# Kernel tuning notes

Hardware: AMD Instinct MI355X
Metric: run time of the kernel (lower is better)

The kernel has to match this reference:

```python
import jax, jax.numpy as jnp
import numpy as np

N_NODES = 100000
FEAT = 256
MAX_DEG = 128
BATCH = 1024
# sampler k uses layer_infos[num_layers-1-k].num_samples: layer_infos num_samples = [25, 10]
NUM_SAMPLES_PER_HOP = [10, 25]
DEPTH = 2


def setup_inputs() -> dict:
    key = jax.random.key(0)
    ks = jax.random.split(key, 10)
    s = 0.05
    return {
        "features": jax.random.normal(ks[0], (N_NODES, FEAT), jnp.float32),
        "w_self_0": jax.random.normal(ks[3], (FEAT, 128), jnp.float32) * s,
        "w_neigh_0": jax.random.normal(ks[4], (FEAT, 128), jnp.float32) * s,
        "w_self_1": jax.random.normal(ks[5], (256, 128), jnp.float32) * s,  # in = 2*128 concat
        "w_neigh_1": jax.random.normal(ks[6], (256, 128), jnp.float32) * s,
        "w_out": jax.random.normal(ks[7], (256, 1), jnp.float32) * s,
        "b_out": jnp.zeros((1,), jnp.float32),
        "node_ids": jax.random.randint(ks[2], (BATCH,), 0, N_NODES, jnp.int32),
        "adj": jax.random.randint(ks[1], (N_NODES, MAX_DEG), 0, N_NODES, jnp.int32),
    }


def _sample(node_ids, adj):
    """Multi-hop uniform neighbor sampling (UniformNeighborSampler chain)."""
    skey = jax.random.key(42)
    samples = [node_ids.reshape(-1)]
    for k, ns in enumerate(NUM_SAMPLES_PER_HOP):
        ids = samples[k]
        rows = jnp.take(adj, ids, axis=0)  # [M, MAX_DEG]
        cols = jax.random.randint(jax.random.fold_in(skey, k), (ids.shape[0], ns), 0, adj.shape[1])
        samples.append(jnp.take_along_axis(rows, cols, axis=1).reshape(-1))
    return samples


def reference(features, w_self_0, w_neigh_0, w_self_1, w_neigh_1, w_out, b_out, node_ids, adj):
    samples = _sample(node_ids, adj)
    hidden = [jnp.take(features, s, axis=0) for s in samples]
    params = [(w_self_0, w_neigh_0), (w_self_1, w_neigh_1)]
    for k in range(DEPTH):
        w_s, w_n = params[k]
        next_hidden = []
        for hop in range(DEPTH - k):
            self_v = hidden[hop]                                   # [M, d]
            neigh = hidden[hop + 1].reshape(self_v.shape[0], NUM_SAMPLES_PER_HOP[hop], -1)
            neigh_mean = neigh.mean(axis=1)                        # [M, d]
            # MeanAggregator, concat=True: relu(concat(self@Ws, mean@Wn))
            next_hidden.append(jax.nn.relu(jnp.concatenate([self_v @ w_s, neigh_mean @ w_n], axis=1)))
        hidden = next_hidden
    h = hidden[0]                                                  # [BATCH, 256]
    h = h / jnp.sqrt(jnp.maximum(jnp.sum(h * h, axis=1, keepdims=True), 1e-12))  # l2_normalize
    return h @ w_out + b_out                                       # Dense(1)
```

## Files before the change

### kernel.cpp

```cpp
#include <hip/hip_runtime.h>
#include <math.h>

struct K2 { unsigned a, b; };

__host__ __device__ constexpr unsigned rotl32c(unsigned x, int r) {
  return (x << r) | (x >> (32 - r));
}

__host__ __device__ constexpr K2 threefry2x32(unsigned k0, unsigned k1,
                                              unsigned x0, unsigned x1) {
  const unsigned ks2 = k0 ^ k1 ^ 0x1BD11BDAu;
  const unsigned ks[3] = {k0, k1, ks2};
  const int rotA[4] = {13, 15, 26, 6};
  const int rotB[4] = {17, 29, 16, 24};
  x0 += k0; x1 += k1;
  for (int g = 0; g < 5; ++g) {
    const int* rr = (g & 1) ? rotB : rotA;
    for (int i = 0; i < 4; ++i) {
      x0 += x1;
      x1 = rotl32c(x1, rr[i]);
      x1 ^= x0;
    }
    x0 += ks[(g + 1) % 3];
    x1 += ks[(g + 2) % 3] + (unsigned)(g + 1);
  }
  return K2{x0, x1};
}

__host__ __device__ constexpr K2 hop_key(unsigned k) {
  K2 f = threefry2x32(0u, 42u, 0u, k);
  return threefry2x32(f.a, f.b, 0u, 1u);
}

constexpr K2 HK0 = hop_key(0u);
constexpr K2 HK1 = hop_key(1u);

__global__ __launch_bounds__(256) void sample_hop1(
    const int* __restrict__ ids, const int* __restrict__ adj,
    int* __restrict__ out, int n) {
  int i = blockIdx.x * 256 + threadIdx.x;
  if (i >= n) return;
  K2 r = threefry2x32(HK0.a, HK0.b, 0u, (unsigned)i);
  int col = (int)((r.a ^ r.b) & 127u);
  out[i] = adj[(long long)ids[i / 10] * 128 + col];
}

__global__ __launch_bounds__(256) void sample_mean_hop2(
    const int* __restrict__ s1, const int* __restrict__ adj,
    const float* __restrict__ feat, float* __restrict__ dst) {
  const int m = blockIdx.x * 4 + (threadIdx.x >> 6);
  const int lane = threadIdx.x & 63;

  const int nid = s1[m];
  int srow;
  {
    unsigned i = (unsigned)(m * 25 + (lane < 25 ? lane : 0));
    K2 r = threefry2x32(HK1.a, HK1.b, 0u, i);
    int col = (int)((r.a ^ r.b) & 127u);
    srow = adj[(long long)nid * 128 + col];
  }

  float4 acc = make_float4(0.f, 0.f, 0.f, 0.f);
#pragma unroll
  for (int c = 0; c < 25; c += 5) {
    float4 v[5];
#pragma unroll
    for (int j = 0; j < 5; ++j) {
      long long row = (long long)__shfl(srow, c + j, 64);
      v[j] = *(const float4*)(feat + row * 256 + (lane << 2));
    }
#pragma unroll
    for (int j = 0; j < 5; ++j) {
      acc.x += v[j].x; acc.y += v[j].y; acc.z += v[j].z; acc.w += v[j].w;
    }
  }
  const float invS = 1.f / 25.f;
  acc.x *= invS; acc.y *= invS; acc.z *= invS; acc.w *= invS;
  *(float4*)(dst + (long long)m * 256 + (lane << 2)) = acc;
}

template <int S>
__global__ __launch_bounds__(256) void mean_rows_w(
    const float* __restrict__ src, const int* __restrict__ idx,
    float* __restrict__ dst, float invS) {
  const int m = blockIdx.x * 4 + (threadIdx.x >> 6);
  const int lane = threadIdx.x & 63;
  const long long base = (long long)m * S;

  int srow = 0;
  if (idx) srow = idx[base + (lane < S ? lane : 0)];

  float4 acc = make_float4(0.f, 0.f, 0.f, 0.f);
#pragma unroll
  for (int c = 0; c < S; c += 5) {
    float4 v[5];
#pragma unroll
    for (int j = 0; j < 5; ++j) {
      if (c + j < S) {
        long long row = idx ? (long long)__shfl(srow, c + j, 64) : (base + c + j);
        v[j] = *(const float4*)(src + row * 256 + (lane << 2));
      }
    }
#pragma unroll
    for (int j = 0; j < 5; ++j) {
      if (c + j < S) {
        acc.x += v[j].x; acc.y += v[j].y; acc.z += v[j].z; acc.w += v[j].w;
      }
    }
  }
  acc.x *= invS; acc.y *= invS; acc.z *= invS; acc.w *= invS;
  *(float4*)(dst + (long long)m * 256 + (lane << 2)) = acc;
}

struct GemmCfg {
  const float* A; const int* idx; const float* B; float* C;
  int ccol0; int mtiles;
};
struct GemmCfg4 { GemmCfg c[4]; };

__global__ __launch_bounds__(256) void gemm_relu_multi(GemmCfg4 cfgs) {
  const GemmCfg cfg = cfgs.c[blockIdx.z];
  if ((int)blockIdx.x >= cfg.mtiles) return;

  __shared__ __align__(16) float As[16][68];
  __shared__ __align__(16) float Bs[16][68];

  const int t = threadIdx.x;
  const int tx = t & 15, ty = t >> 4;
  const int brow = blockIdx.x * 64;
  const int bcol = blockIdx.y * 64;

  const int arow = t >> 2;
  const int ak4 = (t & 3) << 2;
  const int grow = brow + arow;
  const long long asrc = cfg.idx ? (long long)cfg.idx[grow] : (long long)grow;
  const float* Ap = cfg.A + asrc * 256 + ak4;
  const float* Bp = cfg.B + (t >> 4) * 128 + bcol + ((t & 15) << 2);
  const int bkk = t >> 4;
  const int bn4 = (t & 15) << 2;

  float acc[4][4] = {{0.f}};

  for (int k0 = 0; k0 < 256; k0 += 16) {
    float4 av = *(const float4*)(Ap + k0);
    float4 bv = *(const float4*)(Bp + (long long)k0 * 128);
    __syncthreads();
    As[ak4 + 0][arow] = av.x;
    As[ak4 + 1][arow] = av.y;
    As[ak4 + 2][arow] = av.z;
    As[ak4 + 3][arow] = av.w;
    Bs[bkk][bn4 + 0] = bv.x;
    Bs[bkk][bn4 + 1] = bv.y;
    Bs[bkk][bn4 + 2] = bv.z;
    Bs[bkk][bn4 + 3] = bv.w;
    __syncthreads();
#pragma unroll
    for (int kk = 0; kk < 16; ++kk) {
      float4 a = *(const float4*)&As[kk][ty << 2];
      float4 b = *(const float4*)&Bs[kk][tx << 2];
      acc[0][0] += a.x * b.x; acc[0][1] += a.x * b.y; acc[0][2] += a.x * b.z; acc[0][3] += a.x * b.w;
      acc[1][0] += a.y * b.x; acc[1][1] += a.y * b.y; acc[1][2] += a.y * b.z; acc[1][3] += a.y * b.w;
      acc[2][0] += a.z * b.x; acc[2][1] += a.z * b.y; acc[2][2] += a.z * b.z; acc[2][3] += a.z * b.w;
      acc[3][0] += a.w * b.x; acc[3][1] += a.w * b.y; acc[3][2] += a.w * b.z; acc[3][3] += a.w * b.w;
    }
  }

#pragma unroll
  for (int i = 0; i < 4; ++i) {
    const int r = brow + (ty << 2) + i;
    float* Cp = cfg.C + (long long)r * 256 + cfg.ccol0 + bcol + (tx << 2);
#pragma unroll
    for (int j = 0; j < 4; ++j) {
      float v = acc[i][j];
      Cp[j] = v > 0.f ? v : 0.f;
    }
  }
}

__global__ __launch_bounds__(256) void final_kernel(
    const float* __restrict__ h, const float* __restrict__ w,
    const float* __restrict__ b, float* __restrict__ out) {
  const int m = blockIdx.x;
  const int t = threadIdx.x;
  float v = h[(long long)m * 256 + t];
  float wv = w[t];
  float ss = v * v;
  float dd = v * wv;
  for (int off = 32; off; off >>= 1) {
    ss += __shfl_down(ss, off, 64);
    dd += __shfl_down(dd, off, 64);
  }
  __shared__ float s1[4], s2[4];
  const int wid = t >> 6, lane = t & 63;
  if (lane == 0) { s1[wid] = ss; s2[wid] = dd; }
  __syncthreads();
  if (t == 0) {
    float S = s1[0] + s1[1] + s1[2] + s1[3];
    float D = s2[0] + s2[1] + s2[2] + s2[3];
    float n = sqrtf(fmaxf(S, 1e-12f));
    out[m] = D / n + b[0];
  }
}

extern "C" void kernel_launch(void* const* d_in, const int* in_sizes, int n_in,
                              void* d_out, int out_size, void* d_ws, size_t ws_size,
                              hipStream_t stream) {
  (void)in_sizes; (void)n_in; (void)out_size; (void)ws_size;

  const float* features  = (const float*)d_in[0];
  const float* w_self_0  = (const float*)d_in[1];
  const float* w_neigh_0 = (const float*)d_in[2];
  const float* w_self_1  = (const float*)d_in[3];
  const float* w_neigh_1 = (const float*)d_in[4];
  const float* w_out     = (const float*)d_in[5];
  const float* b_out     = (const float*)d_in[6];
  const int*   node_ids  = (const int*)d_in[7];
  const int*   adj       = (const int*)d_in[8];
  float* out = (float*)d_out;

  char* ws = (char*)d_ws;
  size_t off = 0;
  auto alloc = [&](size_t bytes) -> void* {
    void* p = ws + off;
    off = (off + bytes + 255) & ~(size_t)255;
    return p;
  };
  int*   s1   = (int*)alloc(10240 * sizeof(int));
  float* nm1  = (float*)alloc((size_t)10240 * 256 * 4);
  float* nm0  = (float*)alloc((size_t)1024 * 256 * 4);
  float* out1 = (float*)alloc((size_t)10240 * 256 * 4);
  float* out0 = (float*)alloc((size_t)1024 * 256 * 4);
  float* nml1 = (float*)alloc((size_t)1024 * 256 * 4);
  float* hbuf = (float*)alloc((size_t)1024 * 256 * 4);

  sample_hop1<<<40, 256, 0, stream>>>(node_ids, adj, s1, 10240);

  sample_mean_hop2<<<2560, 256, 0, stream>>>(s1, adj, features, nm1);
  mean_rows_w<10><<<256, 256, 0, stream>>>(features, s1, nm0, 0.1f);

  {
    GemmCfg4 cf;
    cf.c[0] = {features, s1,       w_self_0,  out1, 0,   160};
    cf.c[1] = {nm1,      nullptr,  w_neigh_0, out1, 128, 160};
    cf.c[2] = {features, node_ids, w_self_0,  out0, 0,   16};
    cf.c[3] = {nm0,      nullptr,  w_neigh_0, out0, 128, 16};
    gemm_relu_multi<<<dim3(160, 2, 4), 256, 0, stream>>>(cf);
  }

  mean_rows_w<10><<<256, 256, 0, stream>>>(out1, nullptr, nml1, 0.1f);
  {
    GemmCfg4 cf;
    cf.c[0] = {out0, nullptr, w_self_1,  hbuf, 0,   16};
    cf.c[1] = {nml1, nullptr, w_neigh_1, hbuf, 128, 16};
    cf.c[2] = {nullptr, nullptr, nullptr, nullptr, 0, 0};
    cf.c[3] = {nullptr, nullptr, nullptr, nullptr, 0, 0};
    gemm_relu_multi<<<dim3(16, 2, 2), 256, 0, stream>>>(cf);
  }

  final_kernel<<<1024, 256, 0, stream>>>(hbuf, w_out, b_out, out);
}
```

Measured before the change: 253.2 us.

## Template GEMM tiles, use 128x128 tiles with register prefetch and flattened grid

The fused GEMM kernel is templated on block and thread tile sizes. The big first-layer GEMMs move to 128x128 tiles with 8x8 per-thread outputs, the second layer keeps 64x64. Global loads for the next k-slice are now prefetched into registers while the current slice is computed. The 3D grid is replaced by a flat grid that is split across problem configs, so no blocks exit early. Larger tiles raise data reuse and arithmetic intensity, but they use more registers and give fewer blocks (176) than the GPU's CU count, which risks underfilling the device.

```diff
diff --git a/kernel.cpp b/kernel.cpp
--- a/kernel.cpp
+++ b/kernel.cpp
@@ -114,63 +114,93 @@
 
 struct GemmCfg {
   const float* A; const int* idx; const float* B; float* C;
-  int ccol0; int mtiles;
+  int ccol0; int mtiles; int ntiles;
 };
 struct GemmCfg4 { GemmCfg c[4]; };
 
+template <int BM, int BN, int TM, int TN>
 __global__ __launch_bounds__(256) void gemm_relu_multi(GemmCfg4 cfgs) {
-  const GemmCfg cfg = cfgs.c[blockIdx.z];
-  if ((int)blockIdx.x >= cfg.mtiles) return;
-
-  __shared__ __align__(16) float As[16][68];
-  __shared__ __align__(16) float Bs[16][68];
+  int b = blockIdx.x;
+  int z = 0;
+  while (z < 3 && b >= cfgs.c[z].ntiles) { b -= cfgs.c[z].ntiles; ++z; }
+  const GemmCfg cfg = cfgs.c[z];
+  const int mt = b % cfg.mtiles;
+  const int nt = b / cfg.mtiles;
+
+  __shared__ __align__(16) float As[16][BM + 4];
+  __shared__ __align__(16) float Bs[16][BN + 4];
 
   const int t = threadIdx.x;
   const int tx = t & 15, ty = t >> 4;
-  const int brow = blockIdx.x * 64;
-  const int bcol = blockIdx.y * 64;
-
-  const int arow = t >> 2;
-  const int ak4 = (t & 3) << 2;
-  const int grow = brow + arow;
+
+  constexpr int A4 = BM / 64;
+  constexpr int B4 = BN / 64;
+
+  int arow, akb;
+  if constexpr (BM == 128) { arow = t >> 1; akb = (t & 1) << 3; }
+  else { arow = t >> 2; akb = (t & 3) << 2; }
+  const int grow = mt * BM + arow;
   const long long asrc = cfg.idx ? (long long)cfg.idx[grow] : (long long)grow;
-  const float* Ap = cfg.A + asrc * 256 + ak4;
-  const float* Bp = cfg.B + (t >> 4) * 128 + bcol + ((t & 15) << 2);
+  const float* Ap = cfg.A + asrc * 256 + akb;
+
   const int bkk = t >> 4;
-  const int bn4 = (t & 15) << 2;
-
-  float acc[4][4] = {{0.f}};
+  const int bnb = (t & 15) * (BN / 16);
+  const float* Bp = cfg.B + bkk * 128 + nt * BN + bnb;
+
+  float4 av[A4], bv[B4];
+#pragma unroll
+  for (int u = 0; u < A4; ++u) av[u] = *(const float4*)(Ap + (u << 2));
+#pragma unroll
+  for (int u = 0; u < B4; ++u) bv[u] = *(const float4*)(Bp + (u << 2));
+
+  float acc[TM][TN] = {};
 
   for (int k0 = 0; k0 < 256; k0 += 16) {
-    float4 av = *(const float4*)(Ap + k0);
-    float4 bv = *(const float4*)(Bp + (long long)k0 * 128);
     __syncthreads();
-    As[ak4 + 0][arow] = av.x;
-    As[ak4 + 1][arow] = av.y;
-    As[ak4 + 2][arow] = av.z;
-    As[ak4 + 3][arow] = av.w;
-    Bs[bkk][bn4 + 0] = bv.x;
-    Bs[bkk][bn4 + 1] = bv.y;
-    Bs[bkk][bn4 + 2] = bv.z;
-    Bs[bkk][bn4 + 3] = bv.w;
+#pragma unroll
+    for (int u = 0; u < A4; ++u) {
+      As[akb + (u << 2) + 0][arow] = av[u].x;
+      As[akb + (u << 2) + 1][arow] = av[u].y;
+      As[akb + (u << 2) + 2][arow] = av[u].z;
+      As[akb + (u << 2) + 3][arow] = av[u].w;
+    }
+#pragma unroll
+    for (int u = 0; u < B4; ++u)
+      *(float4*)&Bs[bkk][bnb + (u << 2)] = bv[u];
     __syncthreads();
+
+    if (k0 + 16 < 256) {
+#pragma unroll
+      for (int u = 0; u < A4; ++u)
+        av[u] = *(const float4*)(Ap + k0 + 16 + (u << 2));
+#pragma unroll
+      for (int u = 0; u < B4; ++u)
+        bv[u] = *(const float4*)(Bp + (long long)(k0 + 16) * 128 + (u << 2));
+    }
+
 #pragma unroll
     for (int kk = 0; kk < 16; ++kk) {
-      float4 a = *(const float4*)&As[kk][ty << 2];
-      float4 b = *(const float4*)&Bs[kk][tx << 2];
-      acc[0][0] += a.x * b.x; acc[0][1] += a.x * b.y; acc[0][2] += a.x * b.z; acc[0][3] += a.x * b.w;
-      acc[1][0] += a.y * b.x; acc[1][1] += a.y * b.y; acc[1][2] += a.y * b.z; acc[1][3] += a.y * b.w;
-      acc[2][0] += a.z * b.x; acc[2][1] += a.z * b.y; acc[2][2] += a.z * b.z; acc[2][3] += a.z * b.w;
-      acc[3][0] += a.w * b.x; acc[3][1] += a.w * b.y; acc[3][2] += a.w * b.z; acc[3][3] += a.w * b.w;
-    }
-  }
-
-#pragma unroll
-  for (int i = 0; i < 4; ++i) {
-    const int r = brow + (ty << 2) + i;
-    float* Cp = cfg.C + (long long)r * 256 + cfg.ccol0 + bcol + (tx << 2);
-#pragma unroll
-    for (int j = 0; j < 4; ++j) {
+      float a[TM], bb[TN];
+#pragma unroll
+      for (int u = 0; u < TM; u += 4)
+        *(float4*)&a[u] = *(const float4*)&As[kk][ty * TM + u];
+#pragma unroll
+      for (int u = 0; u < TN; u += 4)
+        *(float4*)&bb[u] = *(const float4*)&Bs[kk][tx * TN + u];
+#pragma unroll
+      for (int i = 0; i < TM; ++i)
+#pragma unroll
+        for (int j = 0; j < TN; ++j)
+          acc[i][j] += a[i] * bb[j];
+    }
+  }
+
+#pragma unroll
+  for (int i = 0; i < TM; ++i) {
+    const int r = mt * BM + ty * TM + i;
+    float* Cp = cfg.C + (long long)r * 256 + cfg.ccol0 + nt * BN + tx * TN;
+#pragma unroll
+    for (int j = 0; j < TN; ++j) {
       float v = acc[i][j];
       Cp[j] = v > 0.f ? v : 0.f;
     }
@@ -240,21 +270,21 @@
 
   {
     GemmCfg4 cf;
-    cf.c[0] = {features, s1,       w_self_0,  out1, 0,   160};
-    cf.c[1] = {nm1,      nullptr,  w_neigh_0, out1, 128, 160};
-    cf.c[2] = {features, node_ids, w_self_0,  out0, 0,   16};
-    cf.c[3] = {nm0,      nullptr,  w_neigh_0, out0, 128, 16};
-    gemm_relu_multi<<<dim3(160, 2, 4), 256, 0, stream>>>(cf);
+    cf.c[0] = {features, s1,       w_self_0,  out1, 0,   80, 80};
+    cf.c[1] = {nm1,      nullptr,  w_neigh_0, out1, 128, 80, 80};
+    cf.c[2] = {features, node_ids, w_self_0,  out0, 0,   8,  8};
+    cf.c[3] = {nm0,      nullptr,  w_neigh_0, out0, 128, 8,  8};
+    gemm_relu_multi<128, 128, 8, 8><<<176, 256, 0, stream>>>(cf);
   }
 
   mean_rows_w<10><<<256, 256, 0, stream>>>(out1, nullptr, nml1, 0.1f);
   {
     GemmCfg4 cf;
-    cf.c[0] = {out0, nullptr, w_self_1,  hbuf, 0,   16};
-    cf.c[1] = {nml1, nullptr, w_neigh_1, hbuf, 128, 16};
-    cf.c[2] = {nullptr, nullptr, nullptr, nullptr, 0, 0};
-    cf.c[3] = {nullptr, nullptr, nullptr, nullptr, 0, 0};
-    gemm_relu_multi<<<dim3(16, 2, 2), 256, 0, stream>>>(cf);
+    cf.c[0] = {out0, nullptr, w_self_1,  hbuf, 0,   16, 32};
+    cf.c[1] = {nml1, nullptr, w_neigh_1, hbuf, 128, 16, 32};
+    cf.c[2] = {nullptr, nullptr, nullptr, nullptr, 0, 1, 0};
+    cf.c[3] = {nullptr, nullptr, nullptr, nullptr, 0, 1, 0};
+    gemm_relu_multi<64, 64, 4, 4><<<64, 256, 0, stream>>>(cf);
   }
 
   final_kernel<<<1024, 256, 0, stream>>>(hbuf, w_out, b_out, out);
```

After: 264.4 us. 1.04x slower.

## Fuse sampling kernels, atomic-mean GEMM epilogue, fused final layer

Applied to the files above, without the earlier changes.

Merges hop-1 sampling, the hop-2 gather-mean and the hop-0 mean into one kernel that also zeroes the layer-1 neighbor-mean buffer. The big layer-0 GEMM now averages its outputs straight into that buffer with scaled atomicAdds, so the out1 intermediate and the separate mean pass are gone. The layer-1 GEMM, l2-normalize and output dot are fused into one kernel, and the GEMM grid is flattened into a 1-D tile list. This removes launches and a 10 MB intermediate round-trip. In exchange it adds atomic contention and order-dependent float sums, and the final kernel runs only 64 blocks.

```diff
diff --git a/kernel.cpp b/kernel.cpp
--- a/kernel.cpp
+++ b/kernel.cpp
@@ -35,111 +35,105 @@
 constexpr K2 HK0 = hop_key(0u);
 constexpr K2 HK1 = hop_key(1u);
 
-__global__ __launch_bounds__(256) void sample_hop1(
-    const int* __restrict__ ids, const int* __restrict__ adj,
-    int* __restrict__ out, int n) {
-  int i = blockIdx.x * 256 + threadIdx.x;
-  if (i >= n) return;
-  K2 r = threefry2x32(HK0.a, HK0.b, 0u, (unsigned)i);
-  int col = (int)((r.a ^ r.b) & 127u);
-  out[i] = adj[(long long)ids[i / 10] * 128 + col];
-}
-
-__global__ __launch_bounds__(256) void sample_mean_hop2(
-    const int* __restrict__ s1, const int* __restrict__ adj,
-    const float* __restrict__ feat, float* __restrict__ dst) {
-  const int m = blockIdx.x * 4 + (threadIdx.x >> 6);
+__global__ __launch_bounds__(256) void sample_means(
+    const int* __restrict__ node_ids, const int* __restrict__ adj,
+    const float* __restrict__ feat, int* __restrict__ s1,
+    float* __restrict__ nm1, float* __restrict__ nm0,
+    float* __restrict__ nml1) {
+  const int blk = blockIdx.x;
+  const int w = threadIdx.x >> 6;
   const int lane = threadIdx.x & 63;
 
-  const int nid = s1[m];
-  int srow;
-  {
-    unsigned i = (unsigned)(m * 25 + (lane < 25 ? lane : 0));
-    K2 r = threefry2x32(HK1.a, HK1.b, 0u, i);
-    int col = (int)((r.a ^ r.b) & 127u);
-    srow = adj[(long long)nid * 128 + col];
-  }
-
-  float4 acc = make_float4(0.f, 0.f, 0.f, 0.f);
-#pragma unroll
-  for (int c = 0; c < 25; c += 5) {
-    float4 v[5];
-#pragma unroll
-    for (int j = 0; j < 5; ++j) {
-      long long row = (long long)__shfl(srow, c + j, 64);
-      v[j] = *(const float4*)(feat + row * 256 + (lane << 2));
-    }
-#pragma unroll
-    for (int j = 0; j < 5; ++j) {
-      acc.x += v[j].x; acc.y += v[j].y; acc.z += v[j].z; acc.w += v[j].w;
-    }
-  }
-  const float invS = 1.f / 25.f;
-  acc.x *= invS; acc.y *= invS; acc.z *= invS; acc.w *= invS;
-  *(float4*)(dst + (long long)m * 256 + (lane << 2)) = acc;
-}
-
-template <int S>
-__global__ __launch_bounds__(256) void mean_rows_w(
-    const float* __restrict__ src, const int* __restrict__ idx,
-    float* __restrict__ dst, float invS) {
-  const int m = blockIdx.x * 4 + (threadIdx.x >> 6);
-  const int lane = threadIdx.x & 63;
-  const long long base = (long long)m * S;
-
-  int srow = 0;
-  if (idx) srow = idx[base + (lane < S ? lane : 0)];
-
-  float4 acc = make_float4(0.f, 0.f, 0.f, 0.f);
-#pragma unroll
-  for (int c = 0; c < S; c += 5) {
-    float4 v[5];
-#pragma unroll
-    for (int j = 0; j < 5; ++j) {
-      if (c + j < S) {
-        long long row = idx ? (long long)__shfl(srow, c + j, 64) : (base + c + j);
-        v[j] = *(const float4*)(src + row * 256 + (lane << 2));
-      }
-    }
-#pragma unroll
-    for (int j = 0; j < 5; ++j) {
-      if (c + j < S) {
+  if (blk < 256) {
+    ((float4*)nml1)[blk * 256 + threadIdx.x] = make_float4(0.f, 0.f, 0.f, 0.f);
+  }
+
+  if (blk < 2560) {
+    const int m = blk * 4 + w;
+    K2 r0 = threefry2x32(HK0.a, HK0.b, 0u, (unsigned)m);
+    const int nid = adj[(long long)node_ids[m / 10] * 128 +
+                        (int)((r0.a ^ r0.b) & 127u)];
+    if (lane == 0) s1[m] = nid;
+    int srow;
+    {
+      unsigned i = (unsigned)(m * 25 + (lane < 25 ? lane : 0));
+      K2 r = threefry2x32(HK1.a, HK1.b, 0u, i);
+      srow = adj[(long long)nid * 128 + (int)((r.a ^ r.b) & 127u)];
+    }
+    float4 acc = make_float4(0.f, 0.f, 0.f, 0.f);
+#pragma unroll
+    for (int c = 0; c < 25; c += 5) {
+      float4 v[5];
+#pragma unroll
+      for (int j = 0; j < 5; ++j) {
+        long long row = (long long)__shfl(srow, c + j, 64);
+        v[j] = *(const float4*)(feat + row * 256 + (lane << 2));
+      }
+#pragma unroll
+      for (int j = 0; j < 5; ++j) {
         acc.x += v[j].x; acc.y += v[j].y; acc.z += v[j].z; acc.w += v[j].w;
       }
     }
-  }
-  acc.x *= invS; acc.y *= invS; acc.z *= invS; acc.w *= invS;
-  *(float4*)(dst + (long long)m * 256 + (lane << 2)) = acc;
+    const float s = 1.f / 25.f;
+    acc.x *= s; acc.y *= s; acc.z *= s; acc.w *= s;
+    *(float4*)(nm1 + (long long)m * 256 + (lane << 2)) = acc;
+  } else {
+    const int m0 = (blk - 2560) * 4 + w;
+    int srow;
+    {
+      int j = lane < 10 ? lane : 0;
+      K2 r = threefry2x32(HK0.a, HK0.b, 0u, (unsigned)(m0 * 10 + j));
+      srow = adj[(long long)node_ids[m0] * 128 + (int)((r.a ^ r.b) & 127u)];
+    }
+    float4 acc = make_float4(0.f, 0.f, 0.f, 0.f);
+#pragma unroll
+    for (int c = 0; c < 10; c += 5) {
+      float4 v[5];
+#pragma unroll
+      for (int j = 0; j < 5; ++j) {
+        long long row = (long long)__shfl(srow, c + j, 64);
+        v[j] = *(const float4*)(feat + row * 256 + (lane << 2));
+      }
+#pragma unroll
+      for (int j = 0; j < 5; ++j) {
+        acc.x += v[j].x; acc.y += v[j].y; acc.z += v[j].z; acc.w += v[j].w;
+      }
+    }
+    acc.x *= 0.1f; acc.y *= 0.1f; acc.z *= 0.1f; acc.w *= 0.1f;
+    *(float4*)(nm0 + (long long)m0 * 256 + (lane << 2)) = acc;
+  }
 }
 
 struct GemmCfg {
   const float* A; const int* idx; const float* B; float* C;
-  int ccol0; int mtiles;
+  int ccol0; int mtiles; int tiles; int mode;
 };
 struct GemmCfg4 { GemmCfg c[4]; };
 
 __global__ __launch_bounds__(256) void gemm_relu_multi(GemmCfg4 cfgs) {
-  const GemmCfg cfg = cfgs.c[blockIdx.z];
-  if ((int)blockIdx.x >= cfg.mtiles) return;
+  int b = blockIdx.x, z = 0;
+  while (z < 3 && b >= cfgs.c[z].tiles) { b -= cfgs.c[z].tiles; ++z; }
+  const GemmCfg cfg = cfgs.c[z];
+  const int mt = b % cfg.mtiles;
+  const int nt = b / cfg.mtiles;
 
   __shared__ __align__(16) float As[16][68];
   __shared__ __align__(16) float Bs[16][68];
 
   const int t = threadIdx.x;
   const int tx = t & 15, ty = t >> 4;
-  const int brow = blockIdx.x * 64;
-  const int bcol = blockIdx.y * 64;
 
   const int arow = t >> 2;
   const int ak4 = (t & 3) << 2;
-  const int grow = brow + arow;
+  const int grow = mt * 64 + arow;
   const long long asrc = cfg.idx ? (long long)cfg.idx[grow] : (long long)grow;
   const float* Ap = cfg.A + asrc * 256 + ak4;
-  const float* Bp = cfg.B + (t >> 4) * 128 + bcol + ((t & 15) << 2);
+
   const int bkk = t >> 4;
   const int bn4 = (t & 15) << 2;
-
-  float acc[4][4] = {{0.f}};
+  const float* Bp = cfg.B + bkk * 128 + nt * 64 + bn4;
+
+  float acc[4][4] = {};
 
   for (int k0 = 0; k0 < 256; k0 += 16) {
     float4 av = *(const float4*)(Ap + k0);
@@ -149,56 +143,121 @@
     As[ak4 + 1][arow] = av.y;
     As[ak4 + 2][arow] = av.z;
     As[ak4 + 3][arow] = av.w;
-    Bs[bkk][bn4 + 0] = bv.x;
-    Bs[bkk][bn4 + 1] = bv.y;
-    Bs[bkk][bn4 + 2] = bv.z;
-    Bs[bkk][bn4 + 3] = bv.w;
+    *(float4*)&Bs[bkk][bn4] = bv;
     __syncthreads();
 #pragma unroll
     for (int kk = 0; kk < 16; ++kk) {
       float4 a = *(const float4*)&As[kk][ty << 2];
-      float4 b = *(const float4*)&Bs[kk][tx << 2];
-      acc[0][0] += a.x * b.x; acc[0][1] += a.x * b.y; acc[0][2] += a.x * b.z; acc[0][3] += a.x * b.w;
-      acc[1][0] += a.y * b.x; acc[1][1] += a.y * b.y; acc[1][2] += a.y * b.z; acc[1][3] += a.y * b.w;
-      acc[2][0] += a.z * b.x; acc[2][1] += a.z * b.y; acc[2][2] += a.z * b.z; acc[2][3] += a.z * b.w;
-      acc[3][0] += a.w * b.x; acc[3][1] += a.w * b.y; acc[3][2] += a.w * b.z; acc[3][3] += a.w * b.w;
-    }
-  }
-
-#pragma unroll
-  for (int i = 0; i < 4; ++i) {
-    const int r = brow + (ty << 2) + i;
-    float* Cp = cfg.C + (long long)r * 256 + cfg.ccol0 + bcol + (tx << 2);
-#pragma unroll
-    for (int j = 0; j < 4; ++j) {
-      float v = acc[i][j];
-      Cp[j] = v > 0.f ? v : 0.f;
-    }
-  }
-}
-
-__global__ __launch_bounds__(256) void final_kernel(
-    const float* __restrict__ h, const float* __restrict__ w,
-    const float* __restrict__ b, float* __restrict__ out) {
-  const int m = blockIdx.x;
+      float4 b4 = *(const float4*)&Bs[kk][tx << 2];
+      acc[0][0] += a.x * b4.x; acc[0][1] += a.x * b4.y; acc[0][2] += a.x * b4.z; acc[0][3] += a.x * b4.w;
+      acc[1][0] += a.y * b4.x; acc[1][1] += a.y * b4.y; acc[1][2] += a.y * b4.z; acc[1][3] += a.y * b4.w;
+      acc[2][0] += a.z * b4.x; acc[2][1] += a.z * b4.y; acc[2][2] += a.z * b4.z; acc[2][3] += a.z * b4.w;
+      acc[3][0] += a.w * b4.x; acc[3][1] += a.w * b4.y; acc[3][2] += a.w * b4.z; acc[3][3] += a.w * b4.w;
+    }
+  }
+
+  if (cfg.mode == 0) {
+#pragma unroll
+    for (int i = 0; i < 4; ++i) {
+      const int r = mt * 64 + (ty << 2) + i;
+      float* Cp = cfg.C + (long long)r * 256 + cfg.ccol0 + nt * 64 + (tx << 2);
+#pragma unroll
+      for (int j = 0; j < 4; ++j) {
+        float v = acc[i][j];
+        Cp[j] = v > 0.f ? v : 0.f;
+      }
+    }
+  } else {
+#pragma unroll
+    for (int i = 0; i < 4; ++i) {
+      const int r = mt * 64 + (ty << 2) + i;
+      float* Cp = cfg.C + (long long)(r / 10) * 256 + cfg.ccol0 + nt * 64 + (tx << 2);
+#pragma unroll
+      for (int j = 0; j < 4; ++j) {
+        float v = acc[i][j];
+        atomicAdd(&Cp[j], (v > 0.f ? v : 0.f) * 0.1f);
+      }
+    }
+  }
+}
+
+__global__ __launch_bounds__(256) void layer1_final(
+    const float* __restrict__ out0, const float* __restrict__ nml1,
+    const float* __restrict__ ws1, const float* __restrict__ wn1,
+    const float* __restrict__ w_out, const float* __restrict__ b_out,
+    float* __restrict__ out) {
+  __shared__ __align__(16) float As[16][520];
+  __shared__ __align__(16) float Bs[16][260];
+  __shared__ __align__(16) float Hs[16][260];
+
   const int t = threadIdx.x;
-  float v = h[(long long)m * 256 + t];
-  float wv = w[t];
-  float ss = v * v;
-  float dd = v * wv;
-  for (int off = 32; off; off >>= 1) {
-    ss += __shfl_down(ss, off, 64);
-    dd += __shfl_down(dd, off, 64);
-  }
-  __shared__ float s1[4], s2[4];
-  const int wid = t >> 6, lane = t & 63;
-  if (lane == 0) { s1[wid] = ss; s2[wid] = dd; }
+  const int r0 = blockIdx.x * 16;
+
+#pragma unroll
+  for (int i = 0; i < 8; ++i) {
+    const int f = t + (i << 8);
+    const int row = f >> 7, c4 = f & 127;
+    const float* src = (c4 < 64)
+        ? out0 + (long long)(r0 + row) * 256 + (c4 << 2)
+        : nml1 + (long long)(r0 + row) * 256 + ((c4 - 64) << 2);
+    *(float4*)&As[row][c4 << 2] = *(const float4*)src;
+  }
+
+  const int m = t >> 4;
+  const int cb = t & 15;
+  const int aoff = (cb < 8) ? 0 : 256;
+
+  const int skk = t >> 4;
+  const int sc = (t & 15) << 4;
+  const float* bbase = (sc < 128) ? ws1 + sc : wn1 + (sc - 128);
+
+  float acc[16] = {};
+
+  for (int k0 = 0; k0 < 256; k0 += 16) {
+    const float* bsrc = bbase + (k0 + skk) * 128;
+    __syncthreads();
+#pragma unroll
+    for (int u = 0; u < 4; ++u)
+      *(float4*)&Bs[skk][sc + (u << 2)] = *(const float4*)(bsrc + (u << 2));
+    __syncthreads();
+#pragma unroll
+    for (int q = 0; q < 16; ++q) {
+      const float a = As[m][aoff + k0 + q];
+#pragma unroll
+      for (int j4 = 0; j4 < 4; ++j4) {
+        float4 b4 = *(const float4*)&Bs[q][(cb << 4) + (j4 << 2)];
+        acc[j4 * 4 + 0] += a * b4.x;
+        acc[j4 * 4 + 1] += a * b4.y;
+        acc[j4 * 4 + 2] += a * b4.z;
+        acc[j4 * 4 + 3] += a * b4.w;
+      }
+    }
+  }
+
+#pragma unroll
+  for (int j4 = 0; j4 < 4; ++j4) {
+    float4 h4;
+    h4.x = fmaxf(acc[j4 * 4 + 0], 0.f);
+    h4.y = fmaxf(acc[j4 * 4 + 1], 0.f);
+    h4.z = fmaxf(acc[j4 * 4 + 2], 0.f);
+    h4.w = fmaxf(acc[j4 * 4 + 3], 0.f);
+    *(float4*)&Hs[m][(cb << 4) + (j4 << 2)] = h4;
+  }
   __syncthreads();
-  if (t == 0) {
-    float S = s1[0] + s1[1] + s1[2] + s1[3];
-    float D = s2[0] + s2[1] + s2[2] + s2[3];
-    float n = sqrtf(fmaxf(S, 1e-12f));
-    out[m] = D / n + b[0];
+
+  const int wv = t >> 6, lane = t & 63;
+  for (int rr = 0; rr < 4; ++rr) {
+    const int row = wv * 4 + rr;
+    float4 h4 = *(const float4*)&Hs[row][lane << 2];
+    float4 w4 = *(const float4*)&w_out[lane << 2];
+    float ss = h4.x * h4.x + h4.y * h4.y + h4.z * h4.z + h4.w * h4.w;
+    float dd = h4.x * w4.x + h4.y * w4.y + h4.z * w4.z + h4.w * w4.w;
+    for (int off = 32; off; off >>= 1) {
+      ss += __shfl_down(ss, off, 64);
+      dd += __shfl_down(dd, off, 64);
+    }
+    if (lane == 0)
+      out[r0 + row] = dd / sqrtf(fmaxf(ss, 1e-12f)) + b_out[0];
   }
 }
 
@@ -228,34 +287,20 @@
   int*   s1   = (int*)alloc(10240 * sizeof(int));
   float* nm1  = (float*)alloc((size_t)10240 * 256 * 4);
   float* nm0  = (float*)alloc((size_t)1024 * 256 * 4);
-  float* out1 = (float*)alloc((size_t)10240 * 256 * 4);
   float* out0 = (float*)alloc((size_t)1024 * 256 * 4);
   float* nml1 = (float*)alloc((size_t)1024 * 256 * 4);
-  float* hbuf = (float*)alloc((size_t)1024 * 256 * 4);
-
-  sample_hop1<<<40, 256, 0, stream>>>(node_ids, adj, s1, 10240);
-
-  sample_mean_hop2<<<2560, 256, 0, stream>>>(s1, adj, features, nm1);
-  mean_rows_w<10><<<256, 256, 0, stream>>>(features, s1, nm0, 0.1f);
+
+  sample_means<<<2816, 256, 0, stream>>>(node_ids, adj, features, s1, nm1, nm0, nml1);
 
   {
     GemmCfg4 cf;
-    cf.c[0] = {features, s1,       w_self_0,  out1, 0,   160};
-    cf.c[1] = {nm1,      nullptr,  w_neigh_0, out1, 128, 160};
-    cf.c[2] = {features, node_ids, w_self_0,  out0, 0,   16};
-    cf.c[3] = {nm0,      nullptr,  w_neigh_0, out0, 128, 16};
-    gemm_relu_multi<<<dim3(160, 2, 4), 256, 0, stream>>>(cf);
-  }
-
-  mean_rows_w<10><<<256, 256, 0, stream>>>(out1, nullptr, nml1, 0.1f);
-  {
-    GemmCfg4 cf;
-    cf.c[0] = {out0, nullptr, w_self_1,  hbuf, 0,   16};
-    cf.c[1] = {nml1, nullptr, w_neigh_1, hbuf, 128, 16};
-    cf.c[2] = {nullptr, nullptr, nullptr, nullptr, 0, 0};
-    cf.c[3] = {nullptr, nullptr, nullptr, nullptr, 0, 0};
-    gemm_relu_multi<<<dim3(16, 2, 2), 256, 0, stream>>>(cf);
-  }
-
-  final_kernel<<<1024, 256, 0, stream>>>(hbuf, w_out, b_out, out);
-}
+    cf.c[0] = {features, s1,       w_self_0,  nml1, 0,   160, 320, 1};
+    cf.c[1] = {nm1,      nullptr,  w_neigh_0, nml1, 128, 160, 320, 1};
+    cf.c[2] = {features, node_ids, w_self_0,  out0, 0,   16,  32,  0};
+    cf.c[3] = {nm0,      nullptr,  w_neigh_0, out0, 128, 16,  32,  0};
+    gemm_relu_multi<<<704, 256, 0, stream>>>(cf);
+  }
+
+  layer1_final<<<64, 256, 0, stream>>>(out0, nml1, w_self_1, w_neigh_1,
+                                       w_out, b_out, out);
+}
```

After: 293.3 us. +15.8%, slower.

## Use bf16 MFMA for first-layer GEMMs with weight pre-transpose fused into sampling

Applied to the files above, without the earlier changes.

Replaces the scalar-FMA shared-memory tiled GEMM for layer 0 with a wave-level kernel using bf16 MFMA 16x16x32 instructions. Activations are converted to bf16 on the fly and the weights are transposed and converted to bf16 in extra blocks of the hop-1 sampling kernel. The goal is to cut compute time on the largest GEMM (about 11k rows). It reduces precision to bf16 inputs and drops shared-memory reuse, so each wave reloads B from global memory or cache.

```diff
diff --git a/kernel.cpp b/kernel.cpp
--- a/kernel.cpp
+++ b/kernel.cpp
@@ -1,4 +1,5 @@
 #include <hip/hip_runtime.h>
+#include <hip/hip_bf16.h>
 #include <math.h>
 
 struct K2 { unsigned a, b; };
@@ -35,14 +36,46 @@
 constexpr K2 HK0 = hop_key(0u);
 constexpr K2 HK1 = hop_key(1u);
 
-__global__ __launch_bounds__(256) void sample_hop1(
+typedef __attribute__((ext_vector_type(8))) short short8v;
+typedef __attribute__((ext_vector_type(4))) float f32x4;
+
+__device__ inline short bf16_of(float f) {
+  __hip_bfloat16 h = __float2bfloat16(f);
+  return __builtin_bit_cast(short, h);
+}
+
+__device__ inline short8v cvt8(float4 a, float4 b) {
+  short8v r;
+  r[0] = bf16_of(a.x); r[1] = bf16_of(a.y); r[2] = bf16_of(a.z); r[3] = bf16_of(a.w);
+  r[4] = bf16_of(b.x); r[5] = bf16_of(b.y); r[6] = bf16_of(b.z); r[7] = bf16_of(b.w);
+  return r;
+}
+
+__global__ __launch_bounds__(256) void sample_hop1_wprep(
     const int* __restrict__ ids, const int* __restrict__ adj,
-    int* __restrict__ out, int n) {
-  int i = blockIdx.x * 256 + threadIdx.x;
-  if (i >= n) return;
-  K2 r = threefry2x32(HK0.a, HK0.b, 0u, (unsigned)i);
-  int col = (int)((r.a ^ r.b) & 127u);
-  out[i] = adj[(long long)ids[i / 10] * 128 + col];
+    int* __restrict__ out,
+    const float* __restrict__ w0, const float* __restrict__ w1,
+    short* __restrict__ Wt0, short* __restrict__ Wt1) {
+  const int blk = blockIdx.x;
+  if (blk < 40) {
+    int i = blk * 256 + threadIdx.x;
+    if (i < 10240) {
+      K2 r = threefry2x32(HK0.a, HK0.b, 0u, (unsigned)i);
+      out[i] = adj[(long long)ids[i / 10] * 128 + (int)((r.a ^ r.b) & 127u)];
+    }
+  } else {
+    int e = (blk - 40) * 256 + threadIdx.x;
+    const int half = e >> 13;
+    const int base = (e & 8191) * 4;
+    const float* W = half ? w1 : w0;
+    short* Wt = half ? Wt1 : Wt0;
+#pragma unroll
+    for (int u = 0; u < 4; ++u) {
+      int rr = base + u;
+      int k = rr >> 7, n = rr & 127;
+      Wt[n * 256 + k] = bf16_of(W[k * 128 + n]);
+    }
+  }
 }
 
 __global__ __launch_bounds__(256) void sample_mean_hop2(
@@ -110,6 +143,59 @@
   }
   acc.x *= invS; acc.y *= invS; acc.z *= invS; acc.w *= invS;
   *(float4*)(dst + (long long)m * 256 + (lane << 2)) = acc;
+}
+
+__global__ __launch_bounds__(256) void gemm_mfma(
+    const float* __restrict__ features, const int* __restrict__ s1,
+    const float* __restrict__ nm1, const int* __restrict__ node_ids,
+    const float* __restrict__ nm0,
+    const short* __restrict__ Wt0, const short* __restrict__ Wt1,
+    float* __restrict__ out1, float* __restrict__ out0) {
+  const int z = blockIdx.z;
+  int wt = blockIdx.x * 4 + (threadIdx.x >> 6);
+  const int lane = threadIdx.x & 63;
+
+  const float* A; const int* idx; const short* Wt; float* C; int ccol0;
+  if (z == 0)      { if (wt >= 1280) return; A = features; idx = s1;       Wt = Wt0; C = out1; ccol0 = 0; }
+  else if (z == 1) { if (wt >= 1280) return; A = nm1;      idx = nullptr;  Wt = Wt1; C = out1; ccol0 = 128; }
+  else {
+    if (wt >= 256) return;
+    if (wt < 128)  { A = features; idx = node_ids; Wt = Wt0; C = out0; ccol0 = 0; }
+    else           { A = nm0;      idx = nullptr;  Wt = Wt1; C = out0; ccol0 = 128; wt -= 128; }
+  }
+
+  const int mtile = wt >> 1;
+  const int n0 = (wt & 1) << 6;
+  const int row16 = lane & 15;
+  const int kb = lane >> 4;
+
+  const int grow = mtile * 16 + row16;
+  const long long arow = idx ? (long long)idx[grow] : (long long)grow;
+  const float* Ap = A + arow * 256 + kb * 8;
+  const short* Bp = Wt + (long long)(n0 + row16) * 256 + kb * 8;
+
+  f32x4 acc[4] = {};
+  for (int k0 = 0; k0 < 256; k0 += 32) {
+    float4 a0 = *(const float4*)(Ap + k0);
+    float4 a1 = *(const float4*)(Ap + k0 + 4);
+    short8v af = cvt8(a0, a1);
+#pragma unroll
+    for (int ns = 0; ns < 4; ++ns) {
+      short8v bf = *(const short8v*)(Bp + ns * 16 * 256 + k0);
+      acc[ns] = __builtin_amdgcn_mfma_f32_16x16x32_bf16(af, bf, acc[ns], 0, 0, 0);
+    }
+  }
+
+  const int orow0 = mtile * 16 + kb * 4;
+#pragma unroll
+  for (int ns = 0; ns < 4; ++ns) {
+    const int col = ccol0 + n0 + ns * 16 + row16;
+#pragma unroll
+    for (int r = 0; r < 4; ++r) {
+      float v = acc[ns][r];
+      C[(long long)(orow0 + r) * 256 + col] = v > 0.f ? v : 0.f;
+    }
+  }
 }
 
 struct GemmCfg {
@@ -232,20 +318,17 @@
   float* out0 = (float*)alloc((size_t)1024 * 256 * 4);
   float* nml1 = (float*)alloc((size_t)1024 * 256 * 4);
   float* hbuf = (float*)alloc((size_t)1024 * 256 * 4);
-
-  sample_hop1<<<40, 256, 0, stream>>>(node_ids, adj, s1, 10240);
+  short* Wt0  = (short*)alloc((size_t)128 * 256 * 2);
+  short* Wt1  = (short*)alloc((size_t)128 * 256 * 2);
+
+  sample_hop1_wprep<<<104, 256, 0, stream>>>(node_ids, adj, s1,
+                                             w_self_0, w_neigh_0, Wt0, Wt1);
 
   sample_mean_hop2<<<2560, 256, 0, stream>>>(s1, adj, features, nm1);
   mean_rows_w<10><<<256, 256, 0, stream>>>(features, s1, nm0, 0.1f);
 
-  {
-    GemmCfg4 cf;
-    cf.c[0] = {features, s1,       w_self_0,  out1, 0,   160};
-    cf.c[1] = {nm1,      nullptr,  w_neigh_0, out1, 128, 160};
-    cf.c[2] = {features, node_ids, w_self_0,  out0, 0,   16};
-    cf.c[3] = {nm0,      nullptr,  w_neigh_0, out0, 128, 16};
-    gemm_relu_multi<<<dim3(160, 2, 4), 256, 0, stream>>>(cf);
-  }
+  gemm_mfma<<<dim3(320, 1, 3), 256, 0, stream>>>(
+      features, s1, nm1, node_ids, nm0, Wt0, Wt1, out1, out0);
 
   mean_rows_w<10><<<256, 256, 0, stream>>>(out1, nullptr, nml1, 0.1f);
   {
```

New measurement: 242.7 us. -4.2%, faster.
